# Performance work log

Hardware: AMD Instinct MI355X
Metric: run time of the kernel (lower is better)

## Reference

```python
import jax, jax.numpy as jnp
from jax import lax
import numpy as np

HEADS = 8
SR = 4  # sr_ratio
LN_EPS = 1e-5


def gaussian_filt(x, kernel_size, sigma):
    # depthwise gaussian blur, x: [B, C, H, W]
    ch = x.shape[1]
    c = jnp.arange(kernel_size, dtype=x.dtype)
    xx = jnp.broadcast_to(c[None, :], (kernel_size, kernel_size))
    yy = xx.T
    mean = (kernel_size - 1) / 2.0
    g = jnp.exp(-((xx - mean) ** 2 + (yy - mean) ** 2) / (2.0 * sigma * sigma))
    g = g / g.sum()  # normalization cancels the 1/(2*pi*var) factor
    kern = jnp.broadcast_to(g[None, None], (ch, 1, kernel_size, kernel_size)).astype(x.dtype)
    p = (kernel_size - 1) // 2
    return lax.conv_general_dilated(
        x, kern, (1, 1), [(p, p), (p, p)],
        dimension_numbers=('NCHW', 'OIHW', 'NCHW'), feature_group_count=ch)


def reconstruct_feature(feature, mask, kernel_size, sigma):
    if kernel_size <= 1:
        return feature
    feature = feature * mask
    out = gaussian_filt(jnp.concatenate([feature, mask], axis=1), kernel_size, sigma)
    f_int = out[:, :-1]
    m_int = out[:, -1:]
    f_int = f_int / (m_int + 1e-6)
    m_bin = (m_int > 0).astype(feature.dtype)
    f_int = f_int * m_bin
    return feature + (1.0 - mask) * f_int


def token2map(x, loc, H, W, kernel_size, sigma):
    # x: [B, N, C], loc: [B, N, 2] in [0,1]
    B, N, C = x.shape
    loc = jnp.clip(loc, 0.0, 1.0) * jnp.array([W - 1, H - 1], dtype=loc.dtype)
    loc = jnp.round(loc).astype(jnp.int32)
    idx = loc[..., 0] + loc[..., 1] * W + (jnp.arange(B, dtype=jnp.int32) * (H * W))[:, None]
    src = jnp.concatenate([x, jnp.ones((B, N, 1), x.dtype)], axis=-1).reshape(B * N, C + 1)
    out = jax.ops.segment_sum(src, idx.reshape(-1), num_segments=B * H * W)
    out = out.reshape(B, H, W, C + 1).transpose(0, 3, 1, 2)  # [B, C+1, H, W]
    feature, mask = out[:, :-1], out[:, -1:]
    feature = feature / (mask + 1e-6)
    mask = (mask > 0).astype(x.dtype)
    feature = feature * mask
    return reconstruct_feature(feature, mask, kernel_size, sigma)


def layer_norm(x, w, b):
    mu = jnp.mean(x, axis=-1, keepdims=True)
    var = jnp.mean((x - mu) ** 2, axis=-1, keepdims=True)
    return (x - mu) * lax.rsqrt(var + LN_EPS) * w + b


def forward(x, x_source, loc_source, conf_source, Wq, Wk, Wv, sr_w, sr_b, ln_w, ln_b, Wp, bp, H, W):
    B, N, C = x.shape
    dh = C // HEADS
    scale = dh ** -0.5
    q = (x @ Wq.T).reshape(B, N, HEADS, dh).transpose(0, 2, 1, 3)  # [B,h,N,dh]
    # token2map + spatial reduction
    xm = token2map(x_source, loc_source, H, W, SR - 1, 2.0)        # [B,C,H,W]
    xs = lax.conv_general_dilated(
        xm, sr_w, (SR, SR), 'VALID',
        dimension_numbers=('NCHW', 'OIHW', 'NCHW')) + sr_b[None, :, None, None]
    xs = xs.reshape(B, C, -1).transpose(0, 2, 1)                   # [B,Ns,C]
    xs = layer_norm(xs, ln_w, ln_b)
    Ns = xs.shape[1]
    k = (xs @ Wk.T).reshape(B, Ns, HEADS, dh).transpose(0, 2, 1, 3)
    v = (xs @ Wv.T).reshape(B, Ns, HEADS, dh).transpose(0, 2, 1, 3)
    attn = jnp.einsum('bhnd,bhmd->bhnm', q, k) * scale             # [B,h,N,Ns]
    attn = attn + conf_source[..., 0][:, None, None, :]            # additive bias
    attn = jax.nn.softmax(attn, axis=-1)
    out = jnp.einsum('bhnm,bhmd->bhnd', attn, v)
    out = out.transpose(0, 2, 1, 3).reshape(B, N, C)
    return out @ Wp.T + bp


def setup_inputs() -> dict:
    key = jax.random.key(0)
    ks = jax.random.split(key, 10)
    B, N, C, Hm = 2, 8192, 256, 128
    Ns = (Hm // SR) * (Hm // SR)
    s = 0.02
    return {
        'x': jax.random.normal(ks[0], (B, N, C), jnp.float32),
        'x_source': jax.random.normal(ks[1], (B, N, C), jnp.float32),
        'loc_source': jax.random.uniform(ks[2], (B, N, 2), jnp.float32),
        'conf_source': jax.random.normal(ks[3], (B, Ns, 1), jnp.float32),
        'Wq': jax.random.normal(ks[4], (C, C), jnp.float32) * s,
        'Wk': jax.random.normal(ks[5], (C, C), jnp.float32) * s,
        'Wv': jax.random.normal(ks[6], (C, C), jnp.float32) * s,
        'sr_w': jax.random.normal(ks[7], (C, C, SR, SR), jnp.float32) * s,
        'sr_b': jnp.zeros((C,), jnp.float32),
        'ln_w': jnp.ones((C,), jnp.float32),
        'ln_b': jnp.zeros((C,), jnp.float32),
        'Wp': jax.random.normal(ks[8], (C, C), jnp.float32) * s,
        'bp': jnp.zeros((C,), jnp.float32),
        'H': Hm,
        'W': Hm,
    }


def reference(x, x_source, loc_source, conf_source, Wq, Wk, Wv, sr_w, sr_b, ln_w, ln_b, Wp, bp, H, W):
    return forward(x, x_source, loc_source, conf_source, Wq, Wk, Wv, sr_w, sr_b, ln_w, ln_b, Wp, bp, H, W)
```

## Files before the change

kernel.cpp:

```cpp
#include <hip/hip_runtime.h>
#include <hip/hip_bf16.h>
#include <cstddef>
#include <cstdint>

#define NTOK 8192
#define CD   256
#define HWPIX 16384
#define WIDTH 128
#define NSEQ 1024

typedef __attribute__((ext_vector_type(8))) short bfrag;
typedef __attribute__((ext_vector_type(4))) float f32x4;
typedef __attribute__((ext_vector_type(4))) unsigned int u32x4;

__device__ inline unsigned short f2bfu(float f) {
    __hip_bfloat16 h = __float2bfloat16(f);
    unsigned short u;
    __builtin_memcpy(&u, &h, 2);
    return u;
}
__device__ inline unsigned int rtn16(float f) {
    unsigned int u = __builtin_bit_cast(unsigned int, f);
    return u + 0x7fffu + ((u >> 16) & 1u);
}
__device__ inline float bits2f(unsigned int u) {
    return __builtin_bit_cast(float, u);
}
__device__ inline void gld16(const unsigned short* g, const unsigned short* l) {
    __builtin_amdgcn_global_load_lds(
        (const __attribute__((address_space(1))) unsigned int*)g,
        (__attribute__((address_space(3))) unsigned int*)l, 16, 0, 0);
}
__device__ inline unsigned int cvtpk(float lo, float hi) {
    unsigned int r;
    asm("v_cvt_pk_bf16_f32 %0, %1, %2" : "=v"(r) : "v"(lo), "v"(hi));
    return r;
}
__device__ inline int kslot(int rin) {
    return (((rin >> 5) * 2 + ((rin >> 2) & 1)) << 4)
         + (((rin >> 3) & 3) << 2) + (rin & 3);
}

__global__ __launch_bounds__(256) void scatter_prep(
        const float* __restrict__ xsrc, const float* __restrict__ loc,
        float* __restrict__ feat, float* __restrict__ maskr,
        const float* __restrict__ srw, const float* __restrict__ Wq,
        const float* __restrict__ Wk, const float* __restrict__ Wv,
        const float* __restrict__ Wp, const float* __restrict__ conf,
        const float* __restrict__ x,
        unsigned short* __restrict__ wTb, unsigned short* __restrict__ wqb,
        unsigned short* __restrict__ wkb, unsigned short* __restrict__ wvb,
        unsigned short* __restrict__ wpb, unsigned short* __restrict__ stg,
        unsigned short* __restrict__ xbf) {
    int gid = blockIdx.x, tid = threadIdx.x;
    if (gid < 16384) {
        int token = gid;
        int b = token >> 13;
        float lx = loc[token * 2 + 0];
        float ly = loc[token * 2 + 1];
        lx = fminf(fmaxf(lx, 0.f), 1.f) * 127.0f;
        ly = fminf(fmaxf(ly, 0.f), 1.f) * 127.0f;
        int ix = __float2int_rn(lx);
        int iy = __float2int_rn(ly);
        int p = b * HWPIX + iy * WIDTH + ix;
        atomicAdd(&feat[(size_t)p * CD + tid], xsrc[(size_t)token * CD + tid]);
        if (tid == 0) atomicAdd(&maskr[p], 1.0f);
    } else if (gid < 20480) {
        int idx = (gid - 16384) * 256 + tid;
        int co = idx >> 12;
        int rest = idx & 4095;
        int k16 = rest >> 8;
        int ci = rest & 255;
        int kh = k16 >> 2, kw = k16 & 3;
        wTb[idx] = f2bfu(srw[(size_t)co * 4096 + ci * 16 + kh * 4 + kw]);
    } else if (gid < 20672) {
        const float* s; unsigned short* d; int base;
        if (gid < 20544)      { s = Wq; d = wqb; base = gid - 20480; }
        else if (gid < 20608) { s = Wk; d = wkb; base = gid - 20544; }
        else                  { s = Wv; d = wvb; base = gid - 20608; }
        int i = (base * 256 + tid) * 4;
        float4 v = *(const float4*)(s + i);
        ushort4 o;
        o.x = f2bfu(v.x); o.y = f2bfu(v.y); o.z = f2bfu(v.z); o.w = f2bfu(v.w);
        *(ushort4*)(d + i) = o;
    } else if (gid < 20928) {
        int n = gid - 20672, t = tid;
        float w = Wp[n * 256 + t];
        unsigned short hu = f2bfu(w);
        float hf = bits2f(((unsigned int)hu) << 16);
        unsigned short lu = f2bfu(w - hf);
        wpb[n * 768 + t]       = hu;
        wpb[n * 768 + 256 + t] = lu;
        wpb[n * 768 + 512 + t] = hu;
    } else if (gid < 20936) {
        int idx = (gid - 20928) * 256 + tid;
        int b = idx >> 10, key = idx & 1023;
        int tile = key >> 6, rin = key & 63;
        int slot = kslot(rin);
        float val = conf[idx] * 1.4426950408889634f;
        #pragma unroll
        for (int h = 0; h < 8; h++)
            *(float*)&stg[((size_t)((b * 8 + h) * 16 + tile)) * 5120
                          + 4864 + slot * 2] = val;
    } else {
        size_t idx = ((size_t)(gid - 20936) * 256 + tid) * 4;
        float4 v = *(const float4*)(x + idx);
        ushort4 o;
        o.x = f2bfu(v.x); o.y = f2bfu(v.y); o.z = f2bfu(v.z); o.w = f2bfu(v.w);
        *(ushort4*)(xbf + idx) = o;
    }
}

__global__ __launch_bounds__(256) void recon_patch(const float* __restrict__ feat,
        const float* __restrict__ maskr, unsigned short* __restrict__ apatch) {
    __shared__ float s_wci[36];
    __shared__ float s_vb[36];
    __shared__ int   s_np[36];
    __shared__ float s_ginv[16];
    __shared__ float s_omb[16];
    int blk = blockIdx.x;
    int b  = blk >> 10;
    int py = (blk >> 5) & 31;
    int px = blk & 31;
    int c = threadIdx.x;
    const float e1 = 0.882496902584595f;
    const float e2 = 0.778800783071405f;
    const float snorm = 1.0f / (1.0f + 4.0f * e1 + 4.0f * e2);
    int y0 = py * 4 - 1, x0 = px * 4 - 1;
    if (c < 36) {
        int ry = c / 6, rx = c % 6;
        int yy = y0 + ry, xx = x0 + rx;
        bool valid = (yy >= 0 && yy <= 127 && xx >= 0 && xx <= 127);
        int yc = min(max(yy, 0), 127), xc = min(max(xx, 0), 127);
        int np_ = b * HWPIX + yc * WIDTH + xc;
        float m = maskr[np_];
        float bin = (m > 0.f) ? 1.f : 0.f;
        float inv = 1.0f / (m + 1e-6f);
        s_wci[c] = valid ? bin * inv : 0.f;
        s_vb[c]  = valid ? bin : 0.f;
        s_np[c]  = np_;
    }
    __syncthreads();
    if (c < 16) {
        int oy = c >> 2, ox = c & 3;
        float gm = 0.f;
        #pragma unroll
        for (int dy = -1; dy <= 1; dy++)
            #pragma unroll
            for (int dx = -1; dx <= 1; dx++) {
                int manh = (dy != 0) + (dx != 0);
                float g = ((manh == 2) ? e2 : (manh == 1) ? e1 : 1.0f) * snorm;
                gm += g * s_vb[(oy + 1 + dy) * 6 + (ox + 1 + dx)];
            }
        s_ginv[c] = (gm > 0.f) ? 1.0f / (gm + 1e-6f) : 0.f;
        s_omb[c]  = 1.0f - s_vb[(oy + 1) * 6 + (ox + 1)];
    }
    float gf[4][4], fcv[4][4];
    #pragma unroll
    for (int oy = 0; oy < 4; oy++)
        #pragma unroll
        for (int ox = 0; ox < 4; ox++) { gf[oy][ox] = 0.f; fcv[oy][ox] = 0.f; }
    #pragma unroll
    for (int ry = 0; ry < 6; ry++) {
        #pragma unroll
        for (int rx = 0; rx < 6; rx++) {
            int j = ry * 6 + rx;
            float f = feat[(size_t)s_np[j] * CD + c] * s_wci[j];
            #pragma unroll
            for (int oy = 0; oy < 4; oy++) {
                int dy = ry - 1 - oy;
                if (dy < -1 || dy > 1) continue;
                #pragma unroll
                for (int ox = 0; ox < 4; ox++) {
                    int dx = rx - 1 - ox;
                    if (dx < -1 || dx > 1) continue;
                    int manh = (dy != 0) + (dx != 0);
                    float g = ((manh == 2) ? e2 : (manh == 1) ? e1 : 1.0f) * snorm;
                    gf[oy][ox] += g * f;
                }
            }
            if (ry >= 1 && ry <= 4 && rx >= 1 && rx <= 4)
                fcv[ry - 1][rx - 1] = f;
        }
    }
    __syncthreads();
    int r = b * 1024 + py * 32 + px;
    size_t base = (size_t)r * 4096 + c;
    #pragma unroll
    for (int oy = 0; oy < 4; oy++)
        #pragma unroll
        for (int ox = 0; ox < 4; ox++) {
            int i = oy * 4 + ox;
            float f_int = gf[oy][ox] * s_ginv[i];
            float res = fcv[oy][ox] + s_omb[i] * f_int;
            apatch[base + (size_t)i * 256] = f2bfu(res);
        }
}

template<int TM>
__device__ __forceinline__ void bgemm_body(
        unsigned short* As, unsigned short* Bs,
        const unsigned short* __restrict__ A,
        const unsigned short* __restrict__ B, const float* __restrict__ bias,
        float* __restrict__ C, unsigned short* __restrict__ dstb,
        int M, int N, int K, int Ka, int kfold, int kSplit, int mode,
        float mult, int bx, int by, int bz) {
    constexpr int WRH = TM / 2;
    constexpr int MI  = WRH / 16;
    int tid = threadIdx.x;
    int wave = tid >> 6, lane = tid & 63, m15 = lane & 15, quad = lane >> 4;
    int wr = (wave >> 1) * WRH, wc = (wave & 1) * 64;
    int m0 = by * TM, n0 = bx * 128;
    int kchunk = K / kSplit, k0 = bz * kchunk;
    int srow = tid >> 2, sko = (tid & 3) * 8;
    f32x4 acc[MI][4];
    #pragma unroll
    for (int i = 0; i < MI; i++)
        #pragma unroll
        for (int j = 0; j < 4; j++) acc[i][j] = (f32x4){0.f, 0.f, 0.f, 0.f};
    const unsigned short* Ag = A + (size_t)(m0 + srow) * Ka + sko;
    const unsigned short* Bg = B + (size_t)(n0 + srow) * K + k0 + sko;
    for (int kk = 0; kk < kchunk; kk += 32) {
        int kl = k0 + kk;
        int ke = (kfold && kl >= kfold) ? kl - kfold : kl;
        bfrag a0 = *(const bfrag*)(Ag + ke);
        bfrag a1;
        if constexpr (TM == 128) a1 = *(const bfrag*)(Ag + (size_t)64 * Ka + ke);
        bfrag b0 = *(const bfrag*)(Bg + kk);
        bfrag b1 = *(const bfrag*)(Bg + (size_t)64 * K + kk);
        __syncthreads();
        *(bfrag*)&As[srow * 32 + sko] = a0;
        if constexpr (TM == 128) *(bfrag*)&As[(srow + 64) * 32 + sko] = a1;
        *(bfrag*)&Bs[srow * 32 + sko] = b0;
        *(bfrag*)&Bs[(srow + 64) * 32 + sko] = b1;
        __syncthreads();
        bfrag af[MI], bfr[4];
        #pragma unroll
        for (int mi = 0; mi < MI; mi++)
            af[mi] = *(const bfrag*)&As[(wr + mi * 16 + m15) * 32 + quad * 8];
        #pragma unroll
        for (int ni = 0; ni < 4; ni++)
            bfr[ni] = *(const bfrag*)&Bs[(wc + ni * 16 + m15) * 32 + quad * 8];
        #pragma unroll
        for (int mi = 0; mi < MI; mi++)
            #pragma unroll
            for (int ni = 0; ni < 4; ni++)
                acc[mi][ni] = __builtin_amdgcn_mfma_f32_16x16x32_bf16(
                                  af[mi], bfr[ni], acc[mi][ni], 0, 0, 0);
    }
    if (mode == 2) {
        #pragma unroll
        for (int mi = 0; mi < MI; mi++) {
            #pragma unroll
            for (int i = 0; i < 4; i++) {
                int row = m0 + wr + mi * 16 + quad * 4 + i;
                int b = row >> 13, r = row & 8191;
                #pragma unroll
                for (int ni = 0; ni < 4; ni++) {
                    int col = n0 + wc + ni * 16 + m15;
                    int h = col >> 5, d = col & 31;
                    size_t di = ((((size_t)(b * 8 + h)) << 13) + r) * 32 + d;
                    dstb[di] = f2bfu(acc[mi][ni][i] * mult);
                }
            }
        }
    } else if (mode == 3) {
        #pragma unroll
        for (int mi = 0; mi < MI; mi++) {
            #pragma unroll
            for (int i = 0; i < 4; i++) {
                int row = m0 + wr + mi * 16 + quad * 4 + i;
                int b = row >> 10, key = row & 1023;
                int tile = key >> 6, rin = key & 63;
                int slot = kslot(rin);
                #pragma unroll
                for (int ni = 0; ni < 4; ni++) {
                    int col = n0 + wc + ni * 16 + m15;
                    unsigned short v = f2bfu(acc[mi][ni][i]);
                    if (col < 256) {
                        int h = col >> 5, d = col & 31;
                        size_t di = ((size_t)((b * 8 + h) * 16 + tile)) * 5120
                                    + slot * 40 + d;
                        dstb[di] = v;
                    } else {
                        int c2 = col - 256;
                        int h = c2 >> 5, d = c2 & 31;
                        size_t di = ((size_t)((b * 8 + h) * 16 + tile)) * 5120
                                    + 2560 + d * 72 + rin;
                        dstb[di] = v;
                    }
                }
            }
        }
    } else if (mode == 4) {
        #pragma unroll
        for (int mi = 0; mi < MI; mi++) {
            #pragma unroll
            for (int i = 0; i < 4; i++) {
                size_t row = ((size_t)bz * M + m0 + wr + mi * 16 + quad * 4 + i) * N;
                #pragma unroll
                for (int ni = 0; ni < 4; ni++) {
                    int col = n0 + wc + ni * 16 + m15;
                    C[row + col] = acc[mi][ni][i];
                }
            }
        }
    } else {
        #pragma unroll
        for (int mi = 0; mi < MI; mi++) {
            #pragma unroll
            for (int i = 0; i < 4; i++) {
                size_t row = (size_t)(m0 + wr + mi * 16 + quad * 4 + i) * N;
                #pragma unroll
                for (int ni = 0; ni < 4; ni++) {
                    int col = n0 + wc + ni * 16 + m15;
                    C[row + col] = acc[mi][ni][i] + (bias ? bias[col] : 0.f);
                }
            }
        }
    }
}

template<int TM>
__global__ __launch_bounds__(256) void bgemm(const unsigned short* A,
        const unsigned short* B, const float* bias,
        float* C, unsigned short* dstb,
        int M, int N, int K, int Ka, int kfold, int kSplit, int mode,
        float mult) {
    __shared__ __align__(16) unsigned short As[128 * 32];
    __shared__ __align__(16) unsigned short Bs[128 * 32];
    bgemm_body<TM>(As, Bs, A, B, bias, C, dstb, M, N, K, Ka, kfold, kSplit,
                   mode, mult, blockIdx.x, blockIdx.y, blockIdx.z);
}

__global__ __launch_bounds__(256) void qkv_fused(const unsigned short* xbf,
        const unsigned short* wqb, const unsigned short* xsbf,
        const unsigned short* wkb, unsigned short* Qbf,
        unsigned short* stg, float SC) {
    __shared__ __align__(16) unsigned short As[128 * 32];
    __shared__ __align__(16) unsigned short Bs[128 * 32];
    int g = blockIdx.x;
    if (g < 512) {
        bgemm_body<64>(As, Bs, xbf, wqb, nullptr, nullptr, Qbf,
                       16384, 256, 256, 256, 0, 1, 2, SC, g & 1, g >> 1, 0);
    } else {
        int g2 = g - 512;
        bgemm_body<64>(As, Bs, xsbf, wkb, nullptr, nullptr, stg,
                       2048, 512, 256, 256, 0, 1, 3, 1.f, g2 & 3, g2 >> 2, 0);
    }
}

__global__ __launch_bounds__(256) void ln_red(const float* __restrict__ part,
        const float* __restrict__ srb, const float* __restrict__ w,
        const float* __restrict__ bvec, unsigned short* __restrict__ outb) {
    int row = blockIdx.x;
    int c = threadIdx.x;
    float v = srb[c];
    #pragma unroll
    for (int z = 0; z < 8; z++)
        v += part[((size_t)z * 2048 + row) * 256 + c];
    __shared__ float red[4];
    float s = v;
    #pragma unroll
    for (int o = 32; o >= 1; o >>= 1) s += __shfl_down(s, o, 64);
    if ((c & 63) == 0) red[c >> 6] = s;
    __syncthreads();
    float mean = (red[0] + red[1] + red[2] + red[3]) * (1.f / 256.f);
    __syncthreads();
    float d = v - mean;
    float s2 = d * d;
    #pragma unroll
    for (int o = 32; o >= 1; o >>= 1) s2 += __shfl_down(s2, o, 64);
    if ((c & 63) == 0) red[c >> 6] = s2;
    __syncthreads();
    float var = (red[0] + red[1] + red[2] + red[3]) * (1.f / 256.f);
    float r = 1.0f / sqrtf(var + 1e-5f);
    outb[(size_t)row * 256 + c] = f2bfu(d * r * w[c] + bvec[c]);
}

__global__ __launch_bounds__(256, 2) void attn_v13(
        const unsigned short* __restrict__ Qb,
        const unsigned short* __restrict__ STG,
        unsigned short* __restrict__ aout) {
    __shared__ __align__(16) unsigned short SB[3][5120];
    int tid  = threadIdx.x;
    int wave = tid >> 6;
    int lane = tid & 63;
    int m15  = lane & 15;
    int quad = lane >> 4;
    int flat = blockIdx.y * 32 + blockIdx.x;
    int j  = flat >> 3;
    int bh = (flat & 7) + ((j >> 5) << 3);
    int b  = bh >> 3;
    int h  = bh & 7;
    int qbase = (j & 31) * 256 + wave * 64;

    const unsigned short* qp = Qb + ((size_t)bh * NTOK + qbase) * 32;
    bfrag Qa[4];
    #pragma unroll
    for (int tq = 0; tq < 4; tq++)
        Qa[tq] = *(const bfrag*)(qp + (tq * 16 + m15) * 32 + quad * 8);
    const unsigned short* sg = STG + (size_t)bh * 16 * 5120;

    bfrag ones;
    #pragma unroll
    for (int i = 0; i < 8; i++) ones[i] = (short)0x3F80;

    f32x4 O[4][2];
    f32x4 Lac[4];
    #pragma unroll
    for (int tq = 0; tq < 4; tq++) {
        O[tq][0] = (f32x4){0.f, 0.f, 0.f, 0.f};
        O[tq][1] = (f32x4){0.f, 0.f, 0.f, 0.f};
        Lac[tq]  = (f32x4){0.f, 0.f, 0.f, 0.f};
    }

    #pragma unroll
    for (int pt = 0; pt < 2; pt++) {
        const unsigned short* g = sg + (size_t)pt * 5120;
        unsigned short* l = &SB[pt][0];
        gld16(g + wave * 512 + lane * 8, l + wave * 512);
        gld16(g + (wave + 4) * 512 + lane * 8, l + (wave + 4) * 512);
        if (wave < 2) gld16(g + (8 + wave) * 512 + lane * 8, l + (8 + wave) * 512);
    }

    int cur = 0;
    for (int t = 0; t < 16; t++) {
        if (t < 15) {
            if (wave < 2) asm volatile("s_waitcnt vmcnt(3)" ::: "memory");
            else          asm volatile("s_waitcnt vmcnt(2)" ::: "memory");
        } else {
            asm volatile("s_waitcnt vmcnt(0)" ::: "memory");
        }
        __builtin_amdgcn_s_barrier();
        __builtin_amdgcn_sched_barrier(0);
        const unsigned short* Ks = &SB[0][0] + cur * 5120;
        const unsigned short* Vs = Ks + 2560;
        const float* Cf = (const float*)(Ks + 4864);
        bfrag kf[4]; f32x4 ccf[4];
        #pragma unroll
        for (int s = 0; s < 4; s++) {
            kf[s]  = *(const bfrag*)&Ks[(s * 16 + m15) * 40 + quad * 8];
            ccf[s] = *(const f32x4*)&Cf[s * 16 + quad * 4];
        }
        if (t < 14) {
            int nxt = cur + 2; if (nxt >= 3) nxt -= 3;
            const unsigned short* g = sg + (size_t)(t + 2) * 5120;
            unsigned short* l = &SB[0][0] + nxt * 5120;
            gld16(g + wave * 512 + lane * 8, l + wave * 512);
            gld16(g + (wave + 4) * 512 + lane * 8, l + (wave + 4) * 512);
            if (wave < 2) gld16(g + (8 + wave) * 512 + lane * 8,
                                l + (8 + wave) * 512);
        }
        bfrag Pb[4][2];
        #pragma unroll
        for (int tq = 0; tq < 4; tq++) {
            f32x4 S[4];
            __builtin_amdgcn_s_setprio(1);
            #pragma unroll
            for (int s = 0; s < 4; s++)
                S[s] = __builtin_amdgcn_mfma_f32_16x16x32_bf16(kf[s], Qa[tq],
                                                               ccf[s], 0, 0, 0);
            __builtin_amdgcn_s_setprio(0);
            float v[4][4];
            #pragma unroll
            for (int s = 0; s < 4; s++)
                #pragma unroll
                for (int r = 0; r < 4; r++)
                    v[s][r] = __builtin_amdgcn_exp2f(S[s][r]);
            #pragma unroll
            for (int k2 = 0; k2 < 2; k2++) {
                u32x4 pw;
                pw[0] = cvtpk(v[2 * k2][0],     v[2 * k2][1]);
                pw[1] = cvtpk(v[2 * k2][2],     v[2 * k2][3]);
                pw[2] = cvtpk(v[2 * k2 + 1][0], v[2 * k2 + 1][1]);
                pw[3] = cvtpk(v[2 * k2 + 1][2], v[2 * k2 + 1][3]);
                Pb[tq][k2] = __builtin_bit_cast(bfrag, pw);
            }
        }
        bfrag vfr[2][2];
        #pragma unroll
        for (int k2 = 0; k2 < 2; k2++)
            #pragma unroll
            for (int dt = 0; dt < 2; dt++)
                vfr[k2][dt] = *(const bfrag*)&Vs[(dt * 16 + m15) * 72 +
                                                 k2 * 32 + quad * 8];
        __builtin_amdgcn_s_setprio(1);
        #pragma unroll
        for (int k2 = 0; k2 < 2; k2++)
            #pragma unroll
            for (int tq = 0; tq < 4; tq++) {
                #pragma unroll
                for (int dt = 0; dt < 2; dt++)
                    O[tq][dt] = __builtin_amdgcn_mfma_f32_16x16x32_bf16(
                                    Pb[tq][k2], vfr[k2][dt], O[tq][dt], 0, 0, 0);
                Lac[tq] = __builtin_amdgcn_mfma_f32_16x16x32_bf16(
                                    Pb[tq][k2], ones, Lac[tq], 0, 0, 0);
            }
        __builtin_amdgcn_s_setprio(0);
        cur = (cur == 2) ? 0 : cur + 1;
    }
    #pragma unroll
    for (int tq = 0; tq < 4; tq++) {
        #pragma unroll
        for (int r = 0; r < 4; r++) {
            float inv = 1.0f / Lac[tq][r];
            int row = b * NTOK + qbase + tq * 16 + quad * 4 + r;
            size_t rb = (size_t)row * 512;
            #pragma unroll
            for (int dt = 0; dt < 2; dt++) {
                float o = O[tq][dt][r] * inv;
                unsigned int hr = rtn16(o);
                unsigned short hu = hr >> 16;
                float hf = bits2f(hr & 0xffff0000u);
                unsigned short lu = rtn16(o - hf) >> 16;
                int col = h * 32 + dt * 16 + m15;
                aout[rb + col]       = hu;
                aout[rb + 256 + col] = lu;
            }
        }
    }
}

extern "C" void kernel_launch(void* const* d_in, const int* in_sizes, int n_in,
                              void* d_out, int out_size, void* d_ws, size_t ws_size,
                              hipStream_t stream) {
    const float* x        = (const float*)d_in[0];
    const float* x_source = (const float*)d_in[1];
    const float* loc      = (const float*)d_in[2];
    const float* conf     = (const float*)d_in[3];
    const float* Wq       = (const float*)d_in[4];
    const float* Wk       = (const float*)d_in[5];
    const float* Wv       = (const float*)d_in[6];
    const float* srw      = (const float*)d_in[7];
    const float* srb      = (const float*)d_in[8];
    const float* lnw      = (const float*)d_in[9];
    const float* lnb      = (const float*)d_in[10];
    const float* Wp       = (const float*)d_in[11];
    const float* bp       = (const float*)d_in[12];
    float* out = (float*)d_out;
    float* ws  = (float*)d_ws;

    float* feat = ws;
    unsigned short* Qbf = (unsigned short*)ws;
    float* maskr = ws + 8388608;
    unsigned short* apatch = (unsigned short*)(ws + 8421376);
    unsigned short* aouts  = (unsigned short*)(ws + 8421376);
    unsigned short* wTb    = (unsigned short*)(ws + 12615680);
    unsigned short* stg  = (unsigned short*)(ws + 14712832);
    unsigned short* wqb  = (unsigned short*)(ws + 15368192);
    unsigned short* wkb  = (unsigned short*)(ws + 15400960);
    unsigned short* wvb  = (unsigned short*)(ws + 15433728);
    unsigned short* wpb  = (unsigned short*)(ws + 15466496);
    unsigned short* xsbf = (unsigned short*)(ws + 16089088);
    unsigned short* xbf  = (unsigned short*)(ws + 16351232);
    float*          part = ws + 18448384;

    const float SC = 0.17677669529663687f * 1.4426950408889634f;

    hipMemsetAsync(feat, 0, (size_t)(8388608 + 32768) * sizeof(float), stream);

    scatter_prep<<<25032, 256, 0, stream>>>(x_source, loc, feat, maskr,
                                            srw, Wq, Wk, Wv, Wp, conf, x,
                                            wTb, wqb, wkb, wvb, wpb, stg, xbf);
    recon_patch<<<2048, 256, 0, stream>>>(feat, maskr, apatch);
    bgemm<64><<<dim3(2, 32, 8), 256, 0, stream>>>(apatch, wTb, nullptr,
                                                  part, nullptr,
                                                  2048, 256, 4096, 4096, 0,
                                                  8, 4, 1.f);
    ln_red<<<2048, 256, 0, stream>>>(part, srb, lnw, lnb, xsbf);
    qkv_fused<<<640, 256, 0, stream>>>(xbf, wqb, xsbf, wkb, Qbf, stg, SC);
    attn_v13<<<dim3(32, 16), 256, 0, stream>>>(Qbf, stg, aouts);
    bgemm<64><<<dim3(2, 256, 1), 256, 0, stream>>>(aouts, wpb, bp,
                                                   out, nullptr,
                                                   16384, 256, 768, 512, 256,
                                                   1, 0, 1.f);
}
```

Measured before the change: 218.4 us.

## Pipeline GEMM k-loop with triple-buffered direct global-to-LDS loads

Replaces the register-staged, two-barrier GEMM mainloop with a three-stage LDS ring filled by direct global-to-LDS loads (gld16), prefetching two k-steps ahead. Waits use explicit vmcnt counts and a single barrier per step, and the MFMA block runs at raised wave priority. This is meant to hide global load latency behind MFMA work in all the GEMM kernels. In exchange it uses more LDS per block (36KB), which can lower occupancy, and it depends on the vmcnt counting and the gld16 helper layout being correct.

```diff
diff --git a/kernel.cpp b/kernel.cpp
--- a/kernel.cpp
+++ b/kernel.cpp
@@ -197,60 +197,73 @@
         }
 }
 
-template<int TM>
-__device__ __forceinline__ void bgemm_body(
-        unsigned short* As, unsigned short* Bs,
+__device__ __forceinline__ void bgemm64_body(
+        unsigned short* SB,
         const unsigned short* __restrict__ A,
         const unsigned short* __restrict__ B, const float* __restrict__ bias,
         float* __restrict__ C, unsigned short* __restrict__ dstb,
         int M, int N, int K, int Ka, int kfold, int kSplit, int mode,
         float mult, int bx, int by, int bz) {
-    constexpr int WRH = TM / 2;
-    constexpr int MI  = WRH / 16;
     int tid = threadIdx.x;
     int wave = tid >> 6, lane = tid & 63, m15 = lane & 15, quad = lane >> 4;
-    int wr = (wave >> 1) * WRH, wc = (wave & 1) * 64;
-    int m0 = by * TM, n0 = bx * 128;
+    int wr = (wave >> 1) * 32, wc = (wave & 1) * 64;
+    int m0 = by * 64, n0 = bx * 128;
     int kchunk = K / kSplit, k0 = bz * kchunk;
+    int nst = kchunk / 32;
     int srow = tid >> 2, sko = (tid & 3) * 8;
-    f32x4 acc[MI][4];
-    #pragma unroll
-    for (int i = 0; i < MI; i++)
+    f32x4 acc[2][4];
+    #pragma unroll
+    for (int i = 0; i < 2; i++)
         #pragma unroll
         for (int j = 0; j < 4; j++) acc[i][j] = (f32x4){0.f, 0.f, 0.f, 0.f};
     const unsigned short* Ag = A + (size_t)(m0 + srow) * Ka + sko;
     const unsigned short* Bg = B + (size_t)(n0 + srow) * K + k0 + sko;
-    for (int kk = 0; kk < kchunk; kk += 32) {
-        int kl = k0 + kk;
+    #pragma unroll
+    for (int pt = 0; pt < 2; pt++) {
+        int kl = k0 + pt * 32;
         int ke = (kfold && kl >= kfold) ? kl - kfold : kl;
-        bfrag a0 = *(const bfrag*)(Ag + ke);
-        bfrag a1;
-        if constexpr (TM == 128) a1 = *(const bfrag*)(Ag + (size_t)64 * Ka + ke);
-        bfrag b0 = *(const bfrag*)(Bg + kk);
-        bfrag b1 = *(const bfrag*)(Bg + (size_t)64 * K + kk);
-        __syncthreads();
-        *(bfrag*)&As[srow * 32 + sko] = a0;
-        if constexpr (TM == 128) *(bfrag*)&As[(srow + 64) * 32 + sko] = a1;
-        *(bfrag*)&Bs[srow * 32 + sko] = b0;
-        *(bfrag*)&Bs[(srow + 64) * 32 + sko] = b1;
-        __syncthreads();
-        bfrag af[MI], bfr[4];
-        #pragma unroll
-        for (int mi = 0; mi < MI; mi++)
-            af[mi] = *(const bfrag*)&As[(wr + mi * 16 + m15) * 32 + quad * 8];
+        unsigned short* l = SB + pt * 6144;
+        gld16(Ag + ke, l + wave * 512);
+        gld16(Bg + pt * 32, l + 2048 + wave * 512);
+        gld16(Bg + (size_t)64 * K + pt * 32, l + 4096 + wave * 512);
+    }
+    int cur = 0;
+    for (int t = 0; t < nst; t++) {
+        if (t < nst - 1) asm volatile("s_waitcnt vmcnt(3)" ::: "memory");
+        else             asm volatile("s_waitcnt vmcnt(0)" ::: "memory");
+        __builtin_amdgcn_s_barrier();
+        __builtin_amdgcn_sched_barrier(0);
+        const unsigned short* SBc = SB + cur * 6144;
+        bfrag af[2], bfr[4];
+        #pragma unroll
+        for (int mi = 0; mi < 2; mi++)
+            af[mi] = *(const bfrag*)&SBc[(wr + mi * 16 + m15) * 32 + quad * 8];
         #pragma unroll
         for (int ni = 0; ni < 4; ni++)
-            bfr[ni] = *(const bfrag*)&Bs[(wc + ni * 16 + m15) * 32 + quad * 8];
-        #pragma unroll
-        for (int mi = 0; mi < MI; mi++)
+            bfr[ni] = *(const bfrag*)&SBc[2048 + (wc + ni * 16 + m15) * 32
+                                          + quad * 8];
+        if (t < nst - 2) {
+            int nxt = cur + 2; if (nxt >= 3) nxt -= 3;
+            int kl = k0 + (t + 2) * 32;
+            int ke = (kfold && kl >= kfold) ? kl - kfold : kl;
+            unsigned short* l = SB + nxt * 6144;
+            gld16(Ag + ke, l + wave * 512);
+            gld16(Bg + (t + 2) * 32, l + 2048 + wave * 512);
+            gld16(Bg + (size_t)64 * K + (t + 2) * 32, l + 4096 + wave * 512);
+        }
+        __builtin_amdgcn_s_setprio(1);
+        #pragma unroll
+        for (int mi = 0; mi < 2; mi++)
             #pragma unroll
             for (int ni = 0; ni < 4; ni++)
                 acc[mi][ni] = __builtin_amdgcn_mfma_f32_16x16x32_bf16(
                                   af[mi], bfr[ni], acc[mi][ni], 0, 0, 0);
+        __builtin_amdgcn_s_setprio(0);
+        cur = (cur == 2) ? 0 : cur + 1;
     }
     if (mode == 2) {
         #pragma unroll
-        for (int mi = 0; mi < MI; mi++) {
+        for (int mi = 0; mi < 2; mi++) {
             #pragma unroll
             for (int i = 0; i < 4; i++) {
                 int row = m0 + wr + mi * 16 + quad * 4 + i;
@@ -266,7 +279,7 @@
         }
     } else if (mode == 3) {
         #pragma unroll
-        for (int mi = 0; mi < MI; mi++) {
+        for (int mi = 0; mi < 2; mi++) {
             #pragma unroll
             for (int i = 0; i < 4; i++) {
                 int row = m0 + wr + mi * 16 + quad * 4 + i;
@@ -294,7 +307,7 @@
         }
     } else if (mode == 4) {
         #pragma unroll
-        for (int mi = 0; mi < MI; mi++) {
+        for (int mi = 0; mi < 2; mi++) {
             #pragma unroll
             for (int i = 0; i < 4; i++) {
                 size_t row = ((size_t)bz * M + m0 + wr + mi * 16 + quad * 4 + i) * N;
@@ -307,7 +320,7 @@
         }
     } else {
         #pragma unroll
-        for (int mi = 0; mi < MI; mi++) {
+        for (int mi = 0; mi < 2; mi++) {
             #pragma unroll
             for (int i = 0; i < 4; i++) {
                 size_t row = (size_t)(m0 + wr + mi * 16 + quad * 4 + i) * N;
@@ -321,32 +334,29 @@
     }
 }
 
-template<int TM>
-__global__ __launch_bounds__(256) void bgemm(const unsigned short* A,
+__global__ __launch_bounds__(256) void bgemm64(const unsigned short* A,
         const unsigned short* B, const float* bias,
         float* C, unsigned short* dstb,
         int M, int N, int K, int Ka, int kfold, int kSplit, int mode,
         float mult) {
-    __shared__ __align__(16) unsigned short As[128 * 32];
-    __shared__ __align__(16) unsigned short Bs[128 * 32];
-    bgemm_body<TM>(As, Bs, A, B, bias, C, dstb, M, N, K, Ka, kfold, kSplit,
-                   mode, mult, blockIdx.x, blockIdx.y, blockIdx.z);
+    __shared__ __align__(16) unsigned short SB[3 * 6144];
+    bgemm64_body(SB, A, B, bias, C, dstb, M, N, K, Ka, kfold, kSplit,
+                 mode, mult, blockIdx.x, blockIdx.y, blockIdx.z);
 }
 
 __global__ __launch_bounds__(256) void qkv_fused(const unsigned short* xbf,
         const unsigned short* wqb, const unsigned short* xsbf,
         const unsigned short* wkb, unsigned short* Qbf,
         unsigned short* stg, float SC) {
-    __shared__ __align__(16) unsigned short As[128 * 32];
-    __shared__ __align__(16) unsigned short Bs[128 * 32];
+    __shared__ __align__(16) unsigned short SB[3 * 6144];
     int g = blockIdx.x;
     if (g < 512) {
-        bgemm_body<64>(As, Bs, xbf, wqb, nullptr, nullptr, Qbf,
-                       16384, 256, 256, 256, 0, 1, 2, SC, g & 1, g >> 1, 0);
+        bgemm64_body(SB, xbf, wqb, nullptr, nullptr, Qbf,
+                     16384, 256, 256, 256, 0, 1, 2, SC, g & 1, g >> 1, 0);
     } else {
         int g2 = g - 512;
-        bgemm_body<64>(As, Bs, xsbf, wkb, nullptr, nullptr, stg,
-                       2048, 512, 256, 256, 0, 1, 3, 1.f, g2 & 3, g2 >> 2, 0);
+        bgemm64_body(SB, xsbf, wkb, nullptr, nullptr, stg,
+                     2048, 512, 256, 256, 0, 1, 3, 1.f, g2 & 3, g2 >> 2, 0);
     }
 }
 
@@ -564,15 +574,15 @@
                                             srw, Wq, Wk, Wv, Wp, conf, x,
                                             wTb, wqb, wkb, wvb, wpb, stg, xbf);
     recon_patch<<<2048, 256, 0, stream>>>(feat, maskr, apatch);
-    bgemm<64><<<dim3(2, 32, 8), 256, 0, stream>>>(apatch, wTb, nullptr,
-                                                  part, nullptr,
-                                                  2048, 256, 4096, 4096, 0,
-                                                  8, 4, 1.f);
+    bgemm64<<<dim3(2, 32, 8), 256, 0, stream>>>(apatch, wTb, nullptr,
+                                                part, nullptr,
+                                                2048, 256, 4096, 4096, 0,
+                                                8, 4, 1.f);
     ln_red<<<2048, 256, 0, stream>>>(part, srb, lnw, lnb, xsbf);
     qkv_fused<<<640, 256, 0, stream>>>(xbf, wqb, xsbf, wkb, Qbf, stg, SC);
     attn_v13<<<dim3(32, 16), 256, 0, stream>>>(Qbf, stg, aouts);
-    bgemm<64><<<dim3(2, 256, 1), 256, 0, stream>>>(aouts, wpb, bp,
-                                                   out, nullptr,
-                                                   16384, 256, 768, 512, 256,
-                                                   1, 0, 1.f);
-}
+    bgemm64<<<dim3(2, 256, 1), 256, 0, stream>>>(aouts, wpb, bp,
+                                                 out, nullptr,
+                                                 16384, 256, 768, 512, 256,
+                                                 1, 0, 1.f);
+}
```

Result: faster. 210.9 us, median of 2 (-3.4%).
